# Kernel tuning notes

Measured on AMD Instinct MI355X. Metric: run time of the kernel, lower is better.

## Reference

```python
import jax, jax.numpy as jnp
import numpy as np

B, C, H, W = 4, 256, 64, 64
NH, NQ, HD, WS = 4, 16, 64, 3   # num_heads, num_queries, head_dim, attn_window_size
PD = NH * HD                    # proj_dim = 256


def setup_inputs() -> dict:
    key = jax.random.key(0)
    ks = jax.random.split(key, 6)
    s = 0.02
    return {
        "x": jax.random.normal(ks[0], (B, C, H, W), jnp.float32),
        "kv_w": jax.random.normal(ks[1], (2 * PD, C), jnp.float32) * s,
        "dot_w": jax.random.normal(ks[2], (NH, NQ, HD), jnp.float32) * s,
        "head_w": jax.random.normal(ks[3], (HD, PD), jnp.float32) * s,
        "head_b": jnp.zeros((HD,), jnp.float32),
        "q_w": jax.random.normal(ks[4], (C, NQ * HD), jnp.float32) * s,
        "q_b": jnp.zeros((C,), jnp.float32),
    }


def _unfold(x, ws):
    """Sliding ws x ws patches over last two dims (stride 1, same padding).
    x: (..., h, w) -> (..., h, w, ws*ws), flattened in (i*ws + j) order
    matching torch's unfold(2).unfold(3)."""
    pad = ws // 2
    padw = [(0, 0)] * (x.ndim - 2) + [(pad, pad), (pad, pad)]
    xp = jnp.pad(x, padw)
    h, w = x.shape[-2], x.shape[-1]
    return jnp.stack(
        [xp[..., i:i + h, j:j + w] for i in range(ws) for j in range(ws)],
        axis=-1,
    )


def reference(x, kv_w, dot_w, head_w, head_b, q_w, q_b):
    b, c, h, w = x.shape
    # kv 1x1 conv, then split into k, v (each proj_dim channels)
    kv = jnp.einsum('oc,bchw->bohw', kv_w, x)
    k, v = jnp.split(kv, 2, axis=1)
    # grouped 1x1 conv: per-head head_dim -> num_queries (NOTE: no scale; the
    # original defines self.scale but never applies it in forward)
    kh = k.reshape(b, NH, HD, h, w)
    attn = jnp.einsum('bndhw,nqd->bnqhw', kh, dot_w)
    # unfold overlapping 3x3 windows (L = ws^2 = 9)
    attn_p = _unfold(attn, WS)                        # (b, n, q, h, w, L)
    v_p = _unfold(v.reshape(b, NH, HD, h, w), WS)     # (b, n, d, h, w, L)
    attn_p = jax.nn.softmax(attn_p, axis=-1)
    # per-pixel weighted sum over the window, arranged as (b, q, n, d, h, w)
    out = jnp.einsum('bnqhwl,bndhwl->bqndhw', attn_p, v_p)
    out = out.reshape(b, NQ, PD, h, w)                # (n d) -> proj_dim channels
    # head_proj: 1x1 conv proj_dim -> head_dim (dropout=0)
    y = jnp.einsum('op,bqphw->bqohw', head_w, out) + head_b[None, None, :, None, None]
    # query_proj: 1x1 conv (k*head_dim) -> dim (dropout=0)
    y = y.reshape(b, NQ * HD, h, w)
    z = jnp.einsum('oc,bchw->bohw', q_w, y) + q_b[None, :, None, None]
    return z
```

## Files before the change

kernel.cpp:

```cpp
#include <hip/hip_runtime.h>
#include <hip/hip_bf16.h>
#include <cstdint>

typedef __hip_bfloat16 bf16;
using bf16x8 = __attribute__((ext_vector_type(8))) short;
using f32x4  = __attribute__((ext_vector_type(4))) float;

#define HW_T 4096
#define B_T  4

__device__ __forceinline__ void async_copy16(const bf16* g, bf16* l) {
    __builtin_amdgcn_global_load_lds(
        (const __attribute__((address_space(1))) void*)g,
        (__attribute__((address_space(3))) void*)l, 16, 0, 0);
}
__device__ __forceinline__ short f2bs(float f) {
    bf16 h = __float2bfloat16(f);
    return *reinterpret_cast<short*>(&h);
}

__global__ __launch_bounds__(256) void fuse_all(
    const float* __restrict__ kv_w, const float* __restrict__ dot_w,
    const float* __restrict__ head_w, const float* __restrict__ q_w,
    bf16* __restrict__ W, bf16* __restrict__ qw_b)
{
    const int rb = blockIdx.x;
    if (rb < 384) {
        const int r = rb, c = threadIdx.x;
        float acc = 0.f;
        if (r < 64) {
            const int n = r >> 4, q = r & 15;
            #pragma unroll 8
            for (int d = 0; d < 64; ++d)
                acc += dot_w[(n * 16 + q) * 64 + d] * kv_w[(size_t)(n * 64 + d) * 256 + c];
        } else if (r < 320) {
            const int rr = r - 64, n = rr >> 6, dh = rr & 63;
            #pragma unroll 8
            for (int dd = 0; dd < 64; ++dd)
                acc += head_w[dh * 256 + n * 64 + dd] * kv_w[(size_t)(256 + n * 64 + dd) * 256 + c];
        }
        W[r * 256 + c] = __float2bfloat16(acc);
    } else {
        const int i = (rb - 384) * 256 + threadIdx.x;
        qw_b[i] = __float2bfloat16(q_w[i]);
    }
}

__global__ __launch_bounds__(256) void gemm_xw(
    const float* __restrict__ x, const bf16* __restrict__ W,
    float* __restrict__ AH)
{
    __shared__ __align__(16) bf16 As[2][4][64][8];
    __shared__ __align__(16) bf16 Bs[2][4][128][8];
    const int tid  = threadIdx.x;
    const int wave = tid >> 6, lane = tid & 63;
    const int m0 = blockIdx.x * 64;
    const int n0 = blockIdx.y * 128;
    const int b  = blockIdx.z;
    const float* xb = x + (size_t)b * 256 * HW_T;

    const int px = tid & 63, c8 = tid >> 6;
    const int fi = lane & 15, quad = lane >> 4;
    const int wn = wave * 32;

    f32x4 acc[4][2] = {};
    float xr[8];

    {
        const float* xp = xb + (size_t)(c8 * 8) * HW_T + m0 + px;
        #pragma unroll
        for (int j = 0; j < 8; ++j) xr[j] = xp[(size_t)j * HW_T];
        #pragma unroll
        for (int i = 0; i < 2; ++i) {
            const int slot = i * 256 + tid;
            const int r = slot & 127, q = slot >> 7;
            async_copy16(W + (size_t)(n0 + r) * 256 + q * 8,
                         &Bs[0][0][0][0] + (size_t)(i * 256 + wave * 64) * 8);
        }
        bf16x8 pk;
        #pragma unroll
        for (int j = 0; j < 8; ++j) pk[j] = f2bs(xr[j]);
        *(bf16x8*)&As[0][c8][px][0] = pk;
    }

    for (int it = 0; it < 8; ++it) {
        const int cur = it & 1;
        __syncthreads();
        if (it < 7) {
            const int k1 = (it + 1) * 32;
            const float* xp = xb + (size_t)(k1 + c8 * 8) * HW_T + m0 + px;
            #pragma unroll
            for (int j = 0; j < 8; ++j) xr[j] = xp[(size_t)j * HW_T];
            #pragma unroll
            for (int i = 0; i < 2; ++i) {
                const int slot = i * 256 + tid;
                const int r = slot & 127, q = slot >> 7;
                async_copy16(W + (size_t)(n0 + r) * 256 + k1 + q * 8,
                             &Bs[cur ^ 1][0][0][0] + (size_t)(i * 256 + wave * 64) * 8);
            }
        }
        bf16x8 af[4], bfr[2];
        #pragma unroll
        for (int i = 0; i < 4; ++i)
            af[i] = *(const bf16x8*)&As[cur][quad][i * 16 + fi][0];
        #pragma unroll
        for (int j = 0; j < 2; ++j)
            bfr[j] = *(const bf16x8*)&Bs[cur][quad][wn + j * 16 + fi][0];
        #pragma unroll
        for (int i = 0; i < 4; ++i)
            #pragma unroll
            for (int j = 0; j < 2; ++j)
                acc[i][j] = __builtin_amdgcn_mfma_f32_16x16x32_bf16(
                    af[i], bfr[j], acc[i][j], 0, 0, 0);
        if (it < 7) {
            bf16x8 pk;
            #pragma unroll
            for (int j = 0; j < 8; ++j) pk[j] = f2bs(xr[j]);
            *(bf16x8*)&As[cur ^ 1][c8][px][0] = pk;
        }
    }

    float* Cp = AH + (size_t)b * HW_T * 384;
    #pragma unroll
    for (int i = 0; i < 4; ++i) {
        const int p = m0 + i * 16 + quad * 4;
        #pragma unroll
        for (int r = 0; r < 4; ++r)
            #pragma unroll
            for (int j = 0; j < 2; ++j)
                Cp[(size_t)(p + r) * 384 + n0 + wn + j * 16 + fi] = acc[i][j][r];
    }
}

__global__ __launch_bounds__(256) void gemm_qy(
    const bf16* __restrict__ Aw, const bf16* __restrict__ y,
    const float* __restrict__ q_b, float* __restrict__ z)
{
    __shared__ __align__(16) bf16 As[2][4][64][8];
    __shared__ __align__(16) bf16 Bs[2][4][128][8];
    const int tid  = threadIdx.x;
    const int wave = tid >> 6, lane = tid & 63;
    const int m0 = blockIdx.x * 64;
    const int n0 = blockIdx.y * 128;
    const int b  = blockIdx.z;
    const bf16* Bp = y + (size_t)b * HW_T * 1024;

    const int fi = lane & 15, quad = lane >> 4;
    const int wn = wave * 32;

    f32x4 acc[4][2] = {};

    {
        async_copy16(Aw + (size_t)(m0 + lane) * 1024 + wave * 8,
                     &As[0][0][0][0] + (size_t)tid * 8);
        #pragma unroll
        for (int i = 0; i < 2; ++i) {
            const int slot = i * 256 + tid;
            const int r = slot & 127, q = slot >> 7;
            async_copy16(Bp + (size_t)(n0 + r) * 1024 + q * 8,
                         &Bs[0][0][0][0] + (size_t)(i * 256 + wave * 64) * 8);
        }
    }
    for (int it = 0; it < 32; ++it) {
        const int cur = it & 1;
        __syncthreads();
        if (it < 31) {
            const int k1 = (it + 1) * 32;
            async_copy16(Aw + (size_t)(m0 + lane) * 1024 + k1 + wave * 8,
                         &As[cur ^ 1][0][0][0] + (size_t)tid * 8);
            #pragma unroll
            for (int i = 0; i < 2; ++i) {
                const int slot = i * 256 + tid;
                const int r = slot & 127, q = slot >> 7;
                async_copy16(Bp + (size_t)(n0 + r) * 1024 + k1 + q * 8,
                             &Bs[cur ^ 1][0][0][0] + (size_t)(i * 256 + wave * 64) * 8);
            }
        }
        bf16x8 af[4], bfr[2];
        #pragma unroll
        for (int i = 0; i < 4; ++i)
            af[i] = *(const bf16x8*)&As[cur][quad][i * 16 + fi][0];
        #pragma unroll
        for (int j = 0; j < 2; ++j)
            bfr[j] = *(const bf16x8*)&Bs[cur][quad][wn + j * 16 + fi][0];
        #pragma unroll
        for (int i = 0; i < 4; ++i)
            #pragma unroll
            for (int j = 0; j < 2; ++j)
                acc[i][j] = __builtin_amdgcn_mfma_f32_16x16x32_bf16(
                    af[i], bfr[j], acc[i][j], 0, 0, 0);
    }

    float* Cp = z + (size_t)b * 256 * HW_T;
    #pragma unroll
    for (int i = 0; i < 4; ++i) {
        const int row0 = m0 + i * 16 + quad * 4;
        #pragma unroll
        for (int r = 0; r < 4; ++r) {
            const float bv = q_b[row0 + r];
            #pragma unroll
            for (int j = 0; j < 2; ++j)
                Cp[(size_t)(row0 + r) * HW_T + n0 + wn + j * 16 + fi] = acc[i][j][r] + bv;
        }
    }
}

__global__ __launch_bounds__(256) void attn_apply(
    const float* __restrict__ AH, const float* __restrict__ head_b,
    bf16* __restrict__ y)
{
    const int wv   = threadIdx.x >> 6;
    const int lane = threadIdx.x & 63;
    const int hw   = blockIdx.x * 4 + wv;
    const int b    = blockIdx.y;
    const int h    = hw >> 6, w = hw & 63;
    __shared__ float P[4][9][64];

    int   off[9];
    float okf[9];
    #pragma unroll
    for (int l = 0; l < 9; ++l) {
        const int i = l / 3, j = l % 3;
        const int hh = h + i - 1, ww = w + j - 1;
        const bool ok = ((unsigned)hh < 64u) && ((unsigned)ww < 64u);
        off[l] = ((b * HW_T) + (ok ? hh : h) * 64 + (ok ? ww : w)) * 384;
        okf[l] = ok ? 1.0f : 0.0f;
    }

    {
        float lg[9];
        #pragma unroll
        for (int l = 0; l < 9; ++l) lg[l] = AH[(size_t)off[l] + lane] * okf[l];
        float m = lg[0];
        #pragma unroll
        for (int l = 1; l < 9; ++l) m = fmaxf(m, lg[l]);
        float e[9], s = 0.f;
        #pragma unroll
        for (int l = 0; l < 9; ++l) { e[l] = __expf(lg[l] - m); s += e[l]; }
        const float inv = 1.0f / s;
        #pragma unroll
        for (int l = 0; l < 9; ++l) P[wv][l][lane] = e[l] * inv * okf[l];
    }
    __syncthreads();

    const int fi = lane & 15, quad = lane >> 4;

    bf16x8 afr;
    #pragma unroll
    for (int j = 0; j < 8; ++j) {
        const int k = quad * 8 + j;
        afr[j] = f2bs(P[wv][k >> 2][(k & 3) * 16 + fi]);
    }

    f32x4 acc[4];
    #pragma unroll
    for (int dt = 0; dt < 4; ++dt) {
        const float hb = head_b[dt * 16 + fi];
        acc[dt][0] = hb; acc[dt][1] = hb; acc[dt][2] = hb; acc[dt][3] = hb;
    }

    #pragma unroll
    for (int dt = 0; dt < 4; ++dt) {
        bf16x8 bfr;
        #pragma unroll
        for (int j = 0; j < 8; ++j) {
            const int k = quad * 8 + j;
            const int l = k >> 2, n = k & 3;
            bfr[j] = f2bs(AH[(size_t)off[l] + 64 + n * 64 + dt * 16 + fi]);
        }
        acc[dt] = __builtin_amdgcn_mfma_f32_16x16x32_bf16(afr, bfr, acc[dt], 0, 0, 0);
    }

    #pragma unroll
    for (int n = 0; n < 4; ++n) {
        float pv[4];
        #pragma unroll
        for (int r = 0; r < 4; ++r) pv[r] = P[wv][8][n * 16 + quad * 4 + r];
        #pragma unroll
        for (int dt = 0; dt < 4; ++dt) {
            const float hval = AH[(size_t)off[8] + 64 + n * 64 + dt * 16 + fi];
            #pragma unroll
            for (int r = 0; r < 4; ++r) acc[dt][r] = fmaf(pv[r], hval, acc[dt][r]);
        }
    }

    bf16* yp = y + ((size_t)b * HW_T + hw) * 1024;
    #pragma unroll
    for (int dt = 0; dt < 4; ++dt)
        #pragma unroll
        for (int r = 0; r < 4; ++r)
            yp[(size_t)(quad * 4 + r) * 64 + dt * 16 + fi] = __float2bfloat16(acc[dt][r]);
}

extern "C" void kernel_launch(void* const* d_in, const int* in_sizes, int n_in,
                              void* d_out, int out_size, void* d_ws, size_t ws_size,
                              hipStream_t stream) {
    (void)in_sizes; (void)n_in; (void)out_size; (void)ws_size;
    const float* x      = (const float*)d_in[0];
    const float* kv_w   = (const float*)d_in[1];
    const float* dot_w  = (const float*)d_in[2];
    const float* head_w = (const float*)d_in[3];
    const float* head_b = (const float*)d_in[4];
    const float* q_w    = (const float*)d_in[5];
    const float* q_b    = (const float*)d_in[6];
    float* z = (float*)d_out;

    char* ws    = (char*)d_ws;
    float* AH   = (float*)ws;
    bf16*  y    = (bf16*) (ws + 25165824);
    bf16*  W    = (bf16*) (ws + 58720256);
    bf16*  qw_b = (bf16*) (ws + 58916864);

    fuse_all<<<dim3(1408), 256, 0, stream>>>(kv_w, dot_w, head_w, q_w, W, qw_b);

    gemm_xw<<<dim3(64, 3, B_T), 256, 0, stream>>>(x, W, AH);

    attn_apply<<<dim3(1024, B_T), 256, 0, stream>>>(AH, head_b, y);

    gemm_qy<<<dim3(4, 32, B_T), 256, 0, stream>>>(qw_b, y, q_b, z);
}
```

Before: 138.4 us.

## Fuse windowed attention with query projection GEMM and store AH in bf16

```diff
diff --git a/kernel.cpp b/kernel.cpp
--- a/kernel.cpp
+++ b/kernel.cpp
@@ -17,6 +17,12 @@
 __device__ __forceinline__ short f2bs(float f) {
     bf16 h = __float2bfloat16(f);
     return *reinterpret_cast<short*>(&h);
+}
+__device__ __forceinline__ float bs2f(short s) {
+    unsigned int u = ((unsigned int)(unsigned short)s) << 16;
+    float f;
+    __builtin_memcpy(&f, &u, 4);
+    return f;
 }
 
 __global__ __launch_bounds__(256) void fuse_all(
@@ -48,7 +54,7 @@
 
 __global__ __launch_bounds__(256) void gemm_xw(
     const float* __restrict__ x, const bf16* __restrict__ W,
-    float* __restrict__ AH)
+    bf16* __restrict__ AH)
 {
     __shared__ __align__(16) bf16 As[2][4][64][8];
     __shared__ __align__(16) bf16 Bs[2][4][128][8];
@@ -120,7 +126,7 @@
         }
     }
 
-    float* Cp = AH + (size_t)b * HW_T * 384;
+    bf16* Cp = AH + (size_t)b * HW_T * 384;
     #pragma unroll
     for (int i = 0; i < 4; ++i) {
         const int p = m0 + i * 16 + quad * 4;
@@ -128,168 +134,147 @@
         for (int r = 0; r < 4; ++r)
             #pragma unroll
             for (int j = 0; j < 2; ++j)
-                Cp[(size_t)(p + r) * 384 + n0 + wn + j * 16 + fi] = acc[i][j][r];
-    }
-}
-
-__global__ __launch_bounds__(256) void gemm_qy(
-    const bf16* __restrict__ Aw, const bf16* __restrict__ y,
-    const float* __restrict__ q_b, float* __restrict__ z)
+                Cp[(size_t)(p + r) * 384 + n0 + wn + j * 16 + fi] =
+                    __float2bfloat16(acc[i][j][r]);
+    }
+}
+
+#define YPAD 1032
+#define ATTN_LDS (64 * YPAD * 2 + 8 * 9 * 64 * 4)
+
+__global__ __launch_bounds__(512) void attn_qy(
+    const bf16* __restrict__ AH, const float* __restrict__ head_b,
+    const bf16* __restrict__ qw, const float* __restrict__ q_b,
+    float* __restrict__ z)
 {
-    __shared__ __align__(16) bf16 As[2][4][64][8];
-    __shared__ __align__(16) bf16 Bs[2][4][128][8];
+    extern __shared__ __align__(16) char smem[];
+    bf16*  yL = (bf16*)smem;
+    float* Pm = (float*)(smem + 64 * YPAD * 2) + (threadIdx.x >> 6) * 9 * 64;
+
     const int tid  = threadIdx.x;
     const int wave = tid >> 6, lane = tid & 63;
-    const int m0 = blockIdx.x * 64;
-    const int n0 = blockIdx.y * 128;
-    const int b  = blockIdx.z;
-    const bf16* Bp = y + (size_t)b * HW_T * 1024;
-
+    const int p0  = blockIdx.x * 64;
+    const int b   = p0 >> 12;
+    const int hw0 = p0 & 4095;
+    const int h   = hw0 >> 6;
     const int fi = lane & 15, quad = lane >> 4;
-    const int wn = wave * 32;
-
-    f32x4 acc[4][2] = {};
-
-    {
-        async_copy16(Aw + (size_t)(m0 + lane) * 1024 + wave * 8,
-                     &As[0][0][0][0] + (size_t)tid * 8);
-        #pragma unroll
-        for (int i = 0; i < 2; ++i) {
-            const int slot = i * 256 + tid;
-            const int r = slot & 127, q = slot >> 7;
-            async_copy16(Bp + (size_t)(n0 + r) * 1024 + q * 8,
-                         &Bs[0][0][0][0] + (size_t)(i * 256 + wave * 64) * 8);
-        }
-    }
-    for (int it = 0; it < 32; ++it) {
-        const int cur = it & 1;
+    const ushort* AHu = (const ushort*)AH;
+
+    float hb[4];
+    #pragma unroll
+    for (int dt = 0; dt < 4; ++dt) hb[dt] = head_b[dt * 16 + fi];
+
+    for (int pi = 0; pi < 8; ++pi) {
+        const int w = wave * 8 + pi;
+        int off[9]; float okf[9];
+        #pragma unroll
+        for (int l = 0; l < 9; ++l) {
+            const int i = l / 3, j = l % 3;
+            const int hh = h + i - 1, ww = w + j - 1;
+            const bool ok = ((unsigned)hh < 64u) && ((unsigned)ww < 64u);
+            off[l] = ((b << 12) + (ok ? hh : h) * 64 + (ok ? ww : w)) * 384;
+            okf[l] = ok ? 1.0f : 0.0f;
+        }
+        {
+            float lg[9];
+            #pragma unroll
+            for (int l = 0; l < 9; ++l)
+                lg[l] = bs2f((short)AHu[(size_t)off[l] + lane]) * okf[l];
+            float m = lg[0];
+            #pragma unroll
+            for (int l = 1; l < 9; ++l) m = fmaxf(m, lg[l]);
+            float e[9], s = 0.f;
+            #pragma unroll
+            for (int l = 0; l < 9; ++l) { e[l] = __expf(lg[l] - m); s += e[l]; }
+            const float inv = 1.0f / s;
+            #pragma unroll
+            for (int l = 0; l < 9; ++l) Pm[l * 64 + lane] = e[l] * inv * okf[l];
+        }
         __syncthreads();
-        if (it < 31) {
-            const int k1 = (it + 1) * 32;
-            async_copy16(Aw + (size_t)(m0 + lane) * 1024 + k1 + wave * 8,
-                         &As[cur ^ 1][0][0][0] + (size_t)tid * 8);
-            #pragma unroll
-            for (int i = 0; i < 2; ++i) {
-                const int slot = i * 256 + tid;
-                const int r = slot & 127, q = slot >> 7;
-                async_copy16(Bp + (size_t)(n0 + r) * 1024 + k1 + q * 8,
-                             &Bs[cur ^ 1][0][0][0] + (size_t)(i * 256 + wave * 64) * 8);
+
+        bf16x8 afr;
+        #pragma unroll
+        for (int j = 0; j < 8; ++j) {
+            const int k = quad * 8 + j;
+            afr[j] = f2bs(Pm[(k >> 2) * 64 + (k & 3) * 16 + fi]);
+        }
+        f32x4 acc[4];
+        #pragma unroll
+        for (int dt = 0; dt < 4; ++dt) {
+            acc[dt][0] = hb[dt]; acc[dt][1] = hb[dt];
+            acc[dt][2] = hb[dt]; acc[dt][3] = hb[dt];
+        }
+        #pragma unroll
+        for (int dt = 0; dt < 4; ++dt) {
+            bf16x8 bfr;
+            #pragma unroll
+            for (int j = 0; j < 8; ++j) {
+                const int k = quad * 8 + j;
+                bfr[j] = (short)AHu[(size_t)off[k >> 2] + 64 + (k & 3) * 64 + dt * 16 + fi];
             }
-        }
-        bf16x8 af[4], bfr[2];
-        #pragma unroll
-        for (int i = 0; i < 4; ++i)
-            af[i] = *(const bf16x8*)&As[cur][quad][i * 16 + fi][0];
-        #pragma unroll
-        for (int j = 0; j < 2; ++j)
-            bfr[j] = *(const bf16x8*)&Bs[cur][quad][wn + j * 16 + fi][0];
-        #pragma unroll
-        for (int i = 0; i < 4; ++i)
-            #pragma unroll
-            for (int j = 0; j < 2; ++j)
-                acc[i][j] = __builtin_amdgcn_mfma_f32_16x16x32_bf16(
-                    af[i], bfr[j], acc[i][j], 0, 0, 0);
-    }
-
-    float* Cp = z + (size_t)b * 256 * HW_T;
+            acc[dt] = __builtin_amdgcn_mfma_f32_16x16x32_bf16(afr, bfr, acc[dt], 0, 0, 0);
+        }
+        #pragma unroll
+        for (int n = 0; n < 4; ++n) {
+            float pv[4];
+            #pragma unroll
+            for (int r = 0; r < 4; ++r) pv[r] = Pm[8 * 64 + n * 16 + quad * 4 + r];
+            #pragma unroll
+            for (int dt = 0; dt < 4; ++dt) {
+                const float hval =
+                    bs2f((short)AHu[(size_t)off[8] + 64 + n * 64 + dt * 16 + fi]);
+                #pragma unroll
+                for (int r = 0; r < 4; ++r) acc[dt][r] = fmaf(pv[r], hval, acc[dt][r]);
+            }
+        }
+        #pragma unroll
+        for (int dt = 0; dt < 4; ++dt)
+            #pragma unroll
+            for (int r = 0; r < 4; ++r)
+                yL[(size_t)w * YPAD + (quad * 4 + r) * 64 + dt * 16 + fi] =
+                    __float2bfloat16(acc[dt][r]);
+    }
+    __syncthreads();
+
+    f32x4 zacc[2][4] = {};
+    bf16x8 af[2], afn[2];
     #pragma unroll
-    for (int i = 0; i < 4; ++i) {
-        const int row0 = m0 + i * 16 + quad * 4;
+    for (int i = 0; i < 2; ++i)
+        af[i] = *(const bf16x8*)&qw[(size_t)(wave * 32 + i * 16 + fi) * 1024 + quad * 8];
+
+    #pragma unroll 2
+    for (int k0 = 0; k0 < 1024; k0 += 32) {
+        if (k0 < 992) {
+            #pragma unroll
+            for (int i = 0; i < 2; ++i)
+                afn[i] = *(const bf16x8*)&qw[(size_t)(wave * 32 + i * 16 + fi) * 1024
+                                             + k0 + 32 + quad * 8];
+        }
+        bf16x8 bfr[4];
+        #pragma unroll
+        for (int j = 0; j < 4; ++j)
+            bfr[j] = *(const bf16x8*)&yL[(size_t)(j * 16 + fi) * YPAD + k0 + quad * 8];
+        #pragma unroll
+        for (int i = 0; i < 2; ++i)
+            #pragma unroll
+            for (int j = 0; j < 4; ++j)
+                zacc[i][j] = __builtin_amdgcn_mfma_f32_16x16x32_bf16(
+                    af[i], bfr[j], zacc[i][j], 0, 0, 0);
+        af[0] = afn[0]; af[1] = afn[1];
+    }
+
+    #pragma unroll
+    for (int i = 0; i < 2; ++i) {
+        const int row0 = wave * 32 + i * 16 + quad * 4;
         #pragma unroll
         for (int r = 0; r < 4; ++r) {
             const float bv = q_b[row0 + r];
             #pragma unroll
-            for (int j = 0; j < 2; ++j)
-                Cp[(size_t)(row0 + r) * HW_T + n0 + wn + j * 16 + fi] = acc[i][j][r] + bv;
-        }
-    }
-}
-
-__global__ __launch_bounds__(256) void attn_apply(
-    const float* __restrict__ AH, const float* __restrict__ head_b,
-    bf16* __restrict__ y)
-{
-    const int wv   = threadIdx.x >> 6;
-    const int lane = threadIdx.x & 63;
-    const int hw   = blockIdx.x * 4 + wv;
-    const int b    = blockIdx.y;
-    const int h    = hw >> 6, w = hw & 63;
-    __shared__ float P[4][9][64];
-
-    int   off[9];
-    float okf[9];
-    #pragma unroll
-    for (int l = 0; l < 9; ++l) {
-        const int i = l / 3, j = l % 3;
-        const int hh = h + i - 1, ww = w + j - 1;
-        const bool ok = ((unsigned)hh < 64u) && ((unsigned)ww < 64u);
-        off[l] = ((b * HW_T) + (ok ? hh : h) * 64 + (ok ? ww : w)) * 384;
-        okf[l] = ok ? 1.0f : 0.0f;
-    }
-
-    {
-        float lg[9];
-        #pragma unroll
-        for (int l = 0; l < 9; ++l) lg[l] = AH[(size_t)off[l] + lane] * okf[l];
-        float m = lg[0];
-        #pragma unroll
-        for (int l = 1; l < 9; ++l) m = fmaxf(m, lg[l]);
-        float e[9], s = 0.f;
-        #pragma unroll
-        for (int l = 0; l < 9; ++l) { e[l] = __expf(lg[l] - m); s += e[l]; }
-        const float inv = 1.0f / s;
-        #pragma unroll
-        for (int l = 0; l < 9; ++l) P[wv][l][lane] = e[l] * inv * okf[l];
-    }
-    __syncthreads();
-
-    const int fi = lane & 15, quad = lane >> 4;
-
-    bf16x8 afr;
-    #pragma unroll
-    for (int j = 0; j < 8; ++j) {
-        const int k = quad * 8 + j;
-        afr[j] = f2bs(P[wv][k >> 2][(k & 3) * 16 + fi]);
-    }
-
-    f32x4 acc[4];
-    #pragma unroll
-    for (int dt = 0; dt < 4; ++dt) {
-        const float hb = head_b[dt * 16 + fi];
-        acc[dt][0] = hb; acc[dt][1] = hb; acc[dt][2] = hb; acc[dt][3] = hb;
-    }
-
-    #pragma unroll
-    for (int dt = 0; dt < 4; ++dt) {
-        bf16x8 bfr;
-        #pragma unroll
-        for (int j = 0; j < 8; ++j) {
-            const int k = quad * 8 + j;
-            const int l = k >> 2, n = k & 3;
-            bfr[j] = f2bs(AH[(size_t)off[l] + 64 + n * 64 + dt * 16 + fi]);
-        }
-        acc[dt] = __builtin_amdgcn_mfma_f32_16x16x32_bf16(afr, bfr, acc[dt], 0, 0, 0);
-    }
-
-    #pragma unroll
-    for (int n = 0; n < 4; ++n) {
-        float pv[4];
-        #pragma unroll
-        for (int r = 0; r < 4; ++r) pv[r] = P[wv][8][n * 16 + quad * 4 + r];
-        #pragma unroll
-        for (int dt = 0; dt < 4; ++dt) {
-            const float hval = AH[(size_t)off[8] + 64 + n * 64 + dt * 16 + fi];
-            #pragma unroll
-            for (int r = 0; r < 4; ++r) acc[dt][r] = fmaf(pv[r], hval, acc[dt][r]);
-        }
-    }
-
-    bf16* yp = y + ((size_t)b * HW_T + hw) * 1024;
-    #pragma unroll
-    for (int dt = 0; dt < 4; ++dt)
-        #pragma unroll
-        for (int r = 0; r < 4; ++r)
-            yp[(size_t)(quad * 4 + r) * 64 + dt * 16 + fi] = __float2bfloat16(acc[dt][r]);
+            for (int j = 0; j < 4; ++j)
+                z[((size_t)(b * 256 + row0 + r)) * HW_T + hw0 + j * 16 + fi] =
+                    zacc[i][j][r] + bv;
+        }
+    }
 }
 
 extern "C" void kernel_launch(void* const* d_in, const int* in_sizes, int n_in,
@@ -306,16 +291,20 @@
     float* z = (float*)d_out;
 
     char* ws    = (char*)d_ws;
-    float* AH   = (float*)ws;
-    bf16*  y    = (bf16*) (ws + 25165824);
-    bf16*  W    = (bf16*) (ws + 58720256);
-    bf16*  qw_b = (bf16*) (ws + 58916864);
+    bf16*  AH   = (bf16*)ws;
+    bf16*  W    = (bf16*)(ws + 12582912);
+    bf16*  qw_b = (bf16*)(ws + 12779520);
+
+    static bool attr_done = []() {
+        hipFuncSetAttribute((const void*)attn_qy,
+                            hipFuncAttributeMaxDynamicSharedMemorySize, ATTN_LDS);
+        return true;
+    }();
+    (void)attr_done;
 
     fuse_all<<<dim3(1408), 256, 0, stream>>>(kv_w, dot_w, head_w, q_w, W, qw_b);
 
     gemm_xw<<<dim3(64, 3, B_T), 256, 0, stream>>>(x, W, AH);
 
-    attn_apply<<<dim3(1024, B_T), 256, 0, stream>>>(AH, head_b, y);
-
-    gemm_qy<<<dim3(4, 32, B_T), 256, 0, stream>>>(qw_b, y, q_b, z);
-}
+    attn_qy<<<dim3(256), 512, ATTN_LDS, stream>>>(AH, head_b, qw_b, q_b, z);
+}
```

Measured after the change: 128.4 us. -7.2%, faster.
